# Optimization experiments

Measured on AMD Instinct MI355X. Metric: run time of the kernel, lower is better.

Reference implementation:

```python
import jax, jax.numpy as jnp
import numpy as np

B, H, S, E = 4, 8, 2048, 640
HD = E // H          # 80
MULT = 6
CHUNK = 128          # chunk size for the chunked-recurrent linear attention

def _alibi_slopes(n):
    # standard ALiBi slopes for power-of-2 n (matches _build_slope_tensor)
    start = 2.0 ** (-(2.0 ** -(np.log2(n) - 3.0)))
    return np.array([start * (start ** i) for i in range(n)], dtype=np.float32)

def setup_inputs() -> dict:
    key = jax.random.key(0)
    ks = jax.random.split(key, 3)
    x = jax.random.normal(ks[0], (B, S, E), jnp.float32)
    W1 = jax.random.normal(ks[1], (HD, MULT * HD), jnp.float32) * 0.05
    b1 = jnp.zeros((MULT * HD,), jnp.float32)
    W2 = jax.random.normal(ks[2], (MULT * HD, HD), jnp.float32) * 0.05
    b2 = jnp.zeros((HD,), jnp.float32)
    gamma = jnp.ones((HD,), jnp.float32)
    beta = jnp.zeros((HD,), jnp.float32)
    slopes = jnp.asarray(_alibi_slopes(H))
    return {"x": x, "W1": W1, "b1": b1, "W2": W2, "b2": b2,
            "gamma": gamma, "beta": beta, "slopes": slopes}

def _ln(x, g, b, eps=1e-5):
    m = x.mean(-1, keepdims=True)
    v = x.var(-1, keepdims=True)
    return (x - m) * jax.lax.rsqrt(v + eps) * g + b

def _lightning_attn(q, k, v, s):
    # linear attention with per-head decay exp(-s*(t-i)), causal, no softmax.
    b, h, n, d = q.shape
    c = CHUNK
    nc = n // c
    t = jnp.arange(c, dtype=q.dtype)
    diff = t[:, None] - t[None, :]
    Dmat = jnp.where(diff >= 0, jnp.exp(-s[:, None, None] * diff), 0.0)  # (h,c,c)
    q_dec = jnp.exp(-s[:, None] * t)        # (h,c): decay of query vs chunk start
    k_dec = jnp.exp(-s[:, None] * (c - t))  # (h,c): decay of key to next chunk start
    blk = jnp.exp(-s * c)                   # (h,): whole-chunk state decay

    def to_chunks(a):
        return a.reshape(b, h, nc, c, d).transpose(2, 0, 1, 3, 4)  # (nc,b,h,c,d)

    qc, kc, vc = to_chunks(q), to_chunks(k), to_chunks(v)

    def step(kv, inp):
        qb, kb, vb = inp                                    # (b,h,c,d)
        sc = jnp.einsum('bhid,bhjd->bhij', qb, kb) * Dmat[None]
        o = jnp.einsum('bhij,bhjd->bhid', sc, vb)           # intra-chunk
        o = o + jnp.einsum('bhid,bhde->bhie', qb * q_dec[None, :, :, None], kv)
        kv = blk[None, :, None, None] * kv + jnp.einsum(
            'bhid,bhie->bhde', kb * k_dec[None, :, :, None], vb)
        return kv, o

    kv0 = jnp.zeros((b, h, d, d), q.dtype)
    _, outs = jax.lax.scan(step, kv0, (qc, kc, vc))          # (nc,b,h,c,d)
    return outs.transpose(1, 2, 0, 3, 4).reshape(b, h, n, d)

def reference(x, W1, b1, W2, b2, gamma, beta, slopes):
    hdn = x.reshape(B, H, S, HD)
    hdn = _ln(hdn, gamma, beta)
    residual = hdn  # fixed residual, per the original forward
    for _ in range(2):
        a = _lightning_attn(hdn, hdn, hdn, slopes)
        hdn = _ln(a + residual, gamma, beta)
        ff = jax.nn.leaky_relu(hdn @ W1 + b1) @ W2 + b2  # dropout = eval identity
        hdn = _ln(ff + residual, gamma, beta)
    return hdn.mean(axis=1)  # mean over heads -> (B, S, HD)
```

## Files before the change

kernel.cpp:

```cpp
#include <hip/hip_runtime.h>
#include <hip/hip_bf16.h>

#define BB 4
#define HH 8
#define SS 2048
#define HD 80
#define CC 128
#define NC 16
#define DH 480
#define NROW (BB*HH*SS)
#define ROWSZ ((size_t)NROW * HD)

typedef unsigned short ushortT;
typedef __attribute__((ext_vector_type(8))) short bfrag;
typedef __attribute__((ext_vector_type(4))) float f4;
typedef __attribute__((ext_vector_type(4))) unsigned int u4;

__device__ __forceinline__ ushortT f2bf(float f) {
    __hip_bfloat16 h = __float2bfloat16(f);
    ushortT u; __builtin_memcpy(&u, &h, 2); return u;
}
__device__ __forceinline__ float bf2f(ushortT u) {
    unsigned int x = ((unsigned int)u) << 16;
    float f; __builtin_memcpy(&f, &x, 4); return f;
}

__global__ __launch_bounds__(256) void k_prep(const float* __restrict__ W1,
                                              const float* __restrict__ W2,
                                              ushortT* __restrict__ W1T,
                                              ushortT* __restrict__ W2T) {
    int idx = blockIdx.x * 256 + threadIdx.x;
    if (idx < 480 * 96) {
        int n = idx / 96, k = idx - n * 96;
        float v = (k < HD) ? W1[k * DH + n] : 0.f;
        W1T[idx] = f2bf(v);
    } else if (idx < 480 * 96 + 80 * 480) {
        int j = idx - 480 * 96;
        int n = j / DH, k = j - n * DH;
        W2T[j] = f2bf(W2[k * HD + n]);
    }
}

__global__ __launch_bounds__(256) void k_ln0(const float* __restrict__ x,
                                             const float* __restrict__ g,
                                             const float* __restrict__ be,
                                             ushortT* __restrict__ hdnb,
                                             float* __restrict__ res) {
    int row  = blockIdx.x * 4 + (threadIdx.x >> 6);
    int lane = threadIdx.x & 63;
    const float* xr = x + (size_t)row * HD;
    float v0 = xr[lane];
    float v1 = (lane < 16) ? xr[64 + lane] : 0.f;
    float s  = v0 + v1;
    float sq = v0 * v0 + v1 * v1;
#pragma unroll
    for (int o = 32; o; o >>= 1) { s += __shfl_xor(s, o); sq += __shfl_xor(sq, o); }
    float m    = s * (1.f / 80.f);
    float var  = sq * (1.f / 80.f) - m * m;
    float rstd = rsqrtf(var + 1e-5f);
    size_t base = (size_t)row * HD;
    float y0 = (v0 - m) * rstd * g[lane] + be[lane];
    hdnb[base + lane] = f2bf(y0); res[base + lane] = y0;
    if (lane < 16) {
        float y1 = (v1 - m) * rstd * g[64 + lane] + be[64 + lane];
        hdnb[base + 64 + lane] = f2bf(y1); res[base + 64 + lane] = y1;
    }
}

__global__ __launch_bounds__(256) void k_attn_a(const ushortT* __restrict__ hdn,
                                                const float* __restrict__ slopes,
                                                float* __restrict__ oin,
                                                float* __restrict__ ckv) {
    __shared__ ushortT Xs[CC * 104];
    __shared__ ushortT SC[CC * 40];
    __shared__ ushortT XT[HD * 136];
    __shared__ float dec[CC];
    __shared__ float sqk[CC];

    int t    = threadIdx.x;
    int wave = t >> 6, lane = t & 63;
    int quad = lane >> 4, ln16 = lane & 15;
    int bk = blockIdx.x;
    int bh = bk >> 4;
    int n  = bk & 15;
    float sl = slopes[bh & 7];

    size_t chunkrow = (size_t)bh * SS + (size_t)n * CC;
    const ushortT* xb = hdn + chunkrow * HD;

    if (t < CC) {
        dec[t] = expf(-sl * (float)t);
        sqk[t] = expf(-0.5f * sl * (float)(CC - t));
    }
    for (int u = t; u < CC * HD; u += 256) {
        int i = u / HD, c = u - i * HD;
        ushortT v = xb[u];
        Xs[i * 104 + c] = v;
        XT[c * 136 + i] = v;
    }
    for (int u = t; u < CC * 16; u += 256) {
        int i = u >> 4, c = u & 15;
        Xs[i * 104 + 80 + c] = 0;
    }
    __syncthreads();

    bfrag a[2][3];
#pragma unroll
    for (int rt = 0; rt < 2; ++rt) {
        int mt = wave + rt * 4;
#pragma unroll
        for (int ks = 0; ks < 3; ++ks)
            a[rt][ks] = *(const bfrag*)&Xs[(mt * 16 + ln16) * 104 + ks * 32 + quad * 8];
    }

    f4 oacc[2][5];
#pragma unroll
    for (int rt = 0; rt < 2; ++rt)
#pragma unroll
        for (int ot = 0; ot < 5; ++ot) oacc[rt][ot] = (f4)0.f;

    for (int jt = 0; jt < 4; ++jt) {
        if (wave + 4 < 2 * jt) continue;
        int j0 = jt * 32;
        bfrag bq[2][3];
#pragma unroll
        for (int nt = 0; nt < 2; ++nt)
#pragma unroll
            for (int ks = 0; ks < 3; ++ks)
                bq[nt][ks] = *(const bfrag*)&Xs[(j0 + nt * 16 + ln16) * 104 + ks * 32 + quad * 8];

#pragma unroll
        for (int rt = 0; rt < 2; ++rt) {
            int mt = wave + rt * 4;
            if (mt < 2 * jt) continue;
            int i_base = mt * 16;
            f4 c0 = (f4)0.f, c1 = (f4)0.f;
#pragma unroll
            for (int ks = 0; ks < 3; ++ks) {
                c0 = __builtin_amdgcn_mfma_f32_16x16x32_bf16(a[rt][ks], bq[0][ks], c0, 0, 0, 0);
                c1 = __builtin_amdgcn_mfma_f32_16x16x32_bf16(a[rt][ks], bq[1][ks], c1, 0, 0, 0);
            }
#pragma unroll
            for (int r = 0; r < 4; ++r) {
                int i = i_base + quad * 4 + r;
                int d0 = i - (j0 + ln16);
                int d1 = d0 - 16;
                float f0 = (d0 >= 0) ? dec[d0] : 0.f;
                float f1 = (d1 >= 0) ? dec[d1] : 0.f;
                SC[i * 40 + ln16]      = f2bf(c0[r] * f0);
                SC[i * 40 + 16 + ln16] = f2bf(c1[r] * f1);
            }
            bfrag a2 = *(const bfrag*)&SC[(i_base + ln16) * 40 + quad * 8];
#pragma unroll
            for (int ot = 0; ot < 5; ++ot) {
                bfrag bv = *(const bfrag*)&XT[(ot * 16 + ln16) * 136 + j0 + quad * 8];
                oacc[rt][ot] = __builtin_amdgcn_mfma_f32_16x16x32_bf16(a2, bv, oacc[rt][ot], 0, 0, 0);
            }
        }
    }

#pragma unroll
    for (int rt = 0; rt < 2; ++rt) {
        int i_base = (wave + rt * 4) * 16;
#pragma unroll
        for (int r = 0; r < 4; ++r) {
            size_t grow = (chunkrow + i_base + quad * 4 + r) * HD;
#pragma unroll
            for (int ot = 0; ot < 5; ++ot)
                oin[grow + ot * 16 + ln16] = oacc[rt][ot][r];
        }
    }

    __syncthreads();
    for (int u = t; u < HD * CC; u += 256) {
        int e = u >> 7, j = u & 127;
        int idx = e * 136 + j;
        XT[idx] = f2bf(bf2f(XT[idx]) * sqk[j]);
    }
    __syncthreads();

    float* kvout = ckv + (size_t)bk * (HD * HD);
    for (int p = wave; p < 25; p += 4) {
        int me = p / 5, ne = p - me * 5;
        f4 c = (f4)0.f;
#pragma unroll
        for (int ks = 0; ks < 4; ++ks) {
            bfrag av = *(const bfrag*)&XT[(me * 16 + ln16) * 136 + ks * 32 + quad * 8];
            bfrag bv = *(const bfrag*)&XT[(ne * 16 + ln16) * 136 + ks * 32 + quad * 8];
            c = __builtin_amdgcn_mfma_f32_16x16x32_bf16(av, bv, c, 0, 0, 0);
        }
#pragma unroll
        for (int r = 0; r < 4; ++r)
            kvout[(me * 16 + quad * 4 + r) * HD + ne * 16 + ln16] = c[r];
    }
}

__global__ __launch_bounds__(256) void k_scan(float* __restrict__ kv,
                                              const float* __restrict__ slopes) {
    int idx = blockIdx.x * 256 + threadIdx.x;
    int bh  = idx / (HD * HD);
    int ed  = idx - bh * (HD * HD);
    float bd = expf(-slopes[bh & 7] * (float)CC);
    size_t base = (size_t)bh * NC * (HD * HD) + ed;
    float st = 0.f;
#pragma unroll
    for (int n = 0; n < NC; ++n) {
        size_t p = base + (size_t)n * (HD * HD);
        float cv = kv[p];
        kv[p] = st;
        st = bd * st + cv;
    }
}

__global__ __launch_bounds__(256) void k_attn_b(const ushortT* __restrict__ hdn_in,
                                                const float* __restrict__ oin,
                                                const float* __restrict__ kvs,
                                                const float* __restrict__ res,
                                                const float* __restrict__ slopes,
                                                const float* __restrict__ g,
                                                const float* __restrict__ be,
                                                ushortT* __restrict__ hdn_out) {
    __shared__ ushortT Qs[CC * 104];
    __shared__ ushortT KVT[80 * 104];

    int t    = threadIdx.x;
    int wave = t >> 6, lane = t & 63;
    int qd   = lane >> 4, ln16 = lane & 15;
    int bk = blockIdx.x;
    int bh = bk >> 4;
    int n  = bk & 15;
    float sl = slopes[bh & 7];

    size_t chunkrow = (size_t)bh * SS + (size_t)n * CC;
    const ushortT* xb = hdn_in + chunkrow * HD;
    const float* KV = kvs + ((size_t)bh * NC + n) * (HD * HD);

    {
        const u4* xin = (const u4*)xb;
        u4* Qs4 = (u4*)Qs;
        for (int u = t; u < CC * 10; u += 256) {
            int i = u / 10, c = u - i * 10;
            Qs4[i * 13 + c] = xin[u];
        }
        for (int u = t; u < CC * 16; u += 256) {
            int i = u >> 4, c = u & 15;
            Qs[i * 104 + 80 + c] = 0;
        }
    }
    for (int u = t; u < HD * HD; u += 256) {
        int e = u / HD, d = u - e * HD;
        KVT[d * 104 + e] = f2bf(KV[u]);
    }
    for (int u = t; u < HD * 16; u += 256) {
        int d = u >> 4, e = u & 15;
        KVT[d * 104 + 80 + e] = 0;
    }
    __syncthreads();

    int m0 = wave * 32;
    bfrag a[2][3];
#pragma unroll
    for (int rt = 0; rt < 2; ++rt)
#pragma unroll
        for (int ks = 0; ks < 3; ++ks)
            a[rt][ks] = *(const bfrag*)&Qs[(m0 + rt * 16 + ln16) * 104 + ks * 32 + qd * 8];

    f4 acc[2][5];
#pragma unroll
    for (int ot = 0; ot < 5; ++ot) {
#pragma unroll
        for (int rt = 0; rt < 2; ++rt) acc[rt][ot] = (f4)0.f;
#pragma unroll
        for (int ks = 0; ks < 3; ++ks) {
            bfrag b = *(const bfrag*)&KVT[(ot * 16 + ln16) * 104 + ks * 32 + qd * 8];
#pragma unroll
            for (int rt = 0; rt < 2; ++rt)
                acc[rt][ot] = __builtin_amdgcn_mfma_f32_16x16x32_bf16(a[rt][ks], b, acc[rt][ot], 0, 0, 0);
        }
    }

#pragma unroll
    for (int rt = 0; rt < 2; ++rt) {
#pragma unroll
        for (int r = 0; r < 4; ++r) {
            int i = m0 + rt * 16 + qd * 4 + r;
            float qdec = expf(-sl * (float)i);
            size_t grow = (chunkrow + i) * HD;
            float tv[5];
            float s = 0.f, sq = 0.f;
#pragma unroll
            for (int ot = 0; ot < 5; ++ot) {
                int col = ot * 16 + ln16;
                tv[ot] = oin[grow + col] + qdec * acc[rt][ot][r] + res[grow + col];
                s += tv[ot]; sq += tv[ot] * tv[ot];
            }
#pragma unroll
            for (int o = 8; o; o >>= 1) { s += __shfl_xor(s, o); sq += __shfl_xor(sq, o); }
            float m    = s * (1.f / 80.f);
            float var  = sq * (1.f / 80.f) - m * m;
            float rstd = rsqrtf(var + 1e-5f);
#pragma unroll
            for (int ot = 0; ot < 5; ++ot) {
                int col = ot * 16 + ln16;
                hdn_out[grow + col] = f2bf((tv[ot] - m) * rstd * g[col] + be[col]);
            }
        }
    }
}

__global__ __launch_bounds__(256, 2) void k_ffn(const ushortT* __restrict__ hdn_in,
                                                const ushortT* __restrict__ W1T,
                                                const float* __restrict__ b1,
                                                const ushortT* __restrict__ W2T,
                                                const float* __restrict__ b2,
                                                const float* __restrict__ res,
                                                const float* __restrict__ g,
                                                const float* __restrict__ be,
                                                ushortT* __restrict__ outb,
                                                float* __restrict__ outf,
                                                int write_f32) {
    __shared__ ushortT Xs[128 * 104];
    __shared__ ushortT WH[128 * 104];
    __shared__ ushortT W2s[80 * 104];

    int t    = threadIdx.x;
    int wave = t >> 6, lane = t & 63;
    int qd   = lane >> 4, ln16 = lane & 15;
    size_t rowbase = (size_t)blockIdx.x * 128;

    {
        const u4* xin = (const u4*)(hdn_in + rowbase * HD);
        u4* Xs4 = (u4*)Xs;
        for (int u = t; u < 128 * 10; u += 256) {
            int i = u / 10, c = u - i * 10;
            Xs4[i * 13 + c] = xin[u];
        }
        for (int u = t; u < 128 * 16; u += 256) {
            int i = u >> 4, c = u & 15;
            Xs[i * 104 + 80 + c] = 0;
        }
    }

    f4 acc[2][5];
#pragma unroll
    for (int rt = 0; rt < 2; ++rt)
#pragma unroll
        for (int ot = 0; ot < 5; ++ot) acc[rt][ot] = (f4)0.f;

    const u4* W1T16 = (const u4*)W1T;
    const u4* W2T16 = (const u4*)W2T;
    u4* WH16  = (u4*)WH;
    u4* W2s16 = (u4*)W2s;

    for (int jt = 0; jt < DH; jt += 96) {
        __syncthreads();
        for (int u = t; u < 96 * 12; u += 256) {
            int n = u / 12, k = u - n * 12;
            WH16[n * 13 + k] = W1T16[(size_t)(jt + n) * 12 + k];
        }
        for (int u = t; u < 80 * 12; u += 256) {
            int n = u / 12, k = u - n * 12;
            W2s16[n * 13 + k] = W2T16[(size_t)n * 60 + (jt >> 3) + k];
        }
        __syncthreads();

        f4 hc[2][6];
#pragma unroll
        for (int rt = 0; rt < 2; ++rt)
#pragma unroll
            for (int nt = 0; nt < 6; ++nt) hc[rt][nt] = (f4)0.f;
#pragma unroll
        for (int ks = 0; ks < 3; ++ks) {
            bfrag a0 = *(const bfrag*)&Xs[((wave * 2 + 0) * 16 + ln16) * 104 + ks * 32 + qd * 8];
            bfrag a1 = *(const bfrag*)&Xs[((wave * 2 + 1) * 16 + ln16) * 104 + ks * 32 + qd * 8];
#pragma unroll
            for (int nt = 0; nt < 6; ++nt) {
                bfrag b = *(const bfrag*)&WH[(nt * 16 + ln16) * 104 + ks * 32 + qd * 8];
                hc[0][nt] = __builtin_amdgcn_mfma_f32_16x16x32_bf16(a0, b, hc[0][nt], 0, 0, 0);
                hc[1][nt] = __builtin_amdgcn_mfma_f32_16x16x32_bf16(a1, b, hc[1][nt], 0, 0, 0);
            }
        }
        __syncthreads();

#pragma unroll
        for (int rt = 0; rt < 2; ++rt) {
            int mrow = (wave * 2 + rt) * 16 + qd * 4;
#pragma unroll
            for (int nt = 0; nt < 6; ++nt) {
                float bv = b1[jt + nt * 16 + ln16];
#pragma unroll
                for (int r = 0; r < 4; ++r) {
                    float v = hc[rt][nt][r] + bv;
                    v = (v > 0.f) ? v : 0.01f * v;
                    WH[(mrow + r) * 104 + nt * 16 + ln16] = f2bf(v);
                }
            }
        }
#pragma unroll
        for (int ks = 0; ks < 3; ++ks) {
            bfrag a0 = *(const bfrag*)&WH[((wave * 2 + 0) * 16 + ln16) * 104 + ks * 32 + qd * 8];
            bfrag a1 = *(const bfrag*)&WH[((wave * 2 + 1) * 16 + ln16) * 104 + ks * 32 + qd * 8];
#pragma unroll
            for (int ot = 0; ot < 5; ++ot) {
                bfrag b = *(const bfrag*)&W2s[(ot * 16 + ln16) * 104 + ks * 32 + qd * 8];
                acc[0][ot] = __builtin_amdgcn_mfma_f32_16x16x32_bf16(a0, b, acc[0][ot], 0, 0, 0);
                acc[1][ot] = __builtin_amdgcn_mfma_f32_16x16x32_bf16(a1, b, acc[1][ot], 0, 0, 0);
            }
        }
    }

#pragma unroll
    for (int rt = 0; rt < 2; ++rt) {
        int mbase = (wave * 2 + rt) * 16 + qd * 4;
#pragma unroll
        for (int r = 0; r < 4; ++r) {
            size_t row = rowbase + mbase + r;
            float tv[5];
            float s = 0.f, sq = 0.f;
#pragma unroll
            for (int ot = 0; ot < 5; ++ot) {
                int col = ot * 16 + ln16;
                tv[ot] = acc[rt][ot][r] + b2[col] + res[row * HD + col];
                s += tv[ot]; sq += tv[ot] * tv[ot];
            }
#pragma unroll
            for (int o = 8; o; o >>= 1) { s += __shfl_xor(s, o); sq += __shfl_xor(sq, o); }
            float m    = s * (1.f / 80.f);
            float var  = sq * (1.f / 80.f) - m * m;
            float rstd = rsqrtf(var + 1e-5f);
            if (write_f32) {
#pragma unroll
                for (int ot = 0; ot < 5; ++ot) {
                    int col = ot * 16 + ln16;
                    outf[row * HD + col] = (tv[ot] - m) * rstd * g[col] + be[col];
                }
            } else {
#pragma unroll
                for (int ot = 0; ot < 5; ++ot) {
                    int col = ot * 16 + ln16;
                    outb[row * HD + col] = f2bf((tv[ot] - m) * rstd * g[col] + be[col]);
                }
            }
        }
    }
}

__global__ __launch_bounds__(256) void k_mean(const float* __restrict__ hdn,
                                              float* __restrict__ out) {
    int idx = blockIdx.x * 256 + threadIdx.x;
    int b   = idx / (SS * HD);
    int sd  = idx - b * (SS * HD);
    float s = 0.f;
#pragma unroll
    for (int h = 0; h < HH; ++h)
        s += hdn[((size_t)(b * HH + h)) * (SS * HD) + sd];
    out[idx] = s * 0.125f;
}

extern "C" void kernel_launch(void* const* d_in, const int* in_sizes, int n_in,
                              void* d_out, int out_size, void* d_ws, size_t ws_size,
                              hipStream_t stream) {
    (void)in_sizes; (void)n_in; (void)out_size; (void)ws_size;
    const float* x      = (const float*)d_in[0];
    const float* W1     = (const float*)d_in[1];
    const float* b1     = (const float*)d_in[2];
    const float* W2     = (const float*)d_in[3];
    const float* b2     = (const float*)d_in[4];
    const float* gamma  = (const float*)d_in[5];
    const float* beta   = (const float*)d_in[6];
    const float* slopes = (const float*)d_in[7];
    float* out = (float*)d_out;
    float* ws  = (float*)d_ws;

    float*   res  = ws;
    ushortT* hdnb = (ushortT*)(ws + ROWSZ);
    float*   oin  = ws + 2 * ROWSZ;
    float*   kv   = ws + 3 * ROWSZ;
    float*   hdnf = ws + 4 * ROWSZ;

    ushortT* W1T = (ushortT*)d_out;
    ushortT* W2T = W1T + 480 * 96;

    k_prep<<<(480 * 96 + 80 * 480 + 255) / 256, 256, 0, stream>>>(W1, W2, W1T, W2T);
    k_ln0<<<NROW / 4, 256, 0, stream>>>(x, gamma, beta, hdnb, res);
    for (int it = 0; it < 2; ++it) {
        k_attn_a<<<BB * HH * NC, 256, 0, stream>>>(hdnb, slopes, oin, kv);
        k_scan<<<(BB * HH * HD * HD) / 256, 256, 0, stream>>>(kv, slopes);
        k_attn_b<<<BB * HH * NC, 256, 0, stream>>>(hdnb, oin, kv, res, slopes, gamma, beta, hdnb);
        k_ffn<<<NROW / 128, 256, 0, stream>>>(hdnb, W1T, b1, W2T, b2, res, gamma, beta,
                                              hdnb, hdnf, (it == 1) ? 1 : 0);
    }
    k_mean<<<(BB * SS * HD) / 256, 256, 0, stream>>>(hdnf, out);
}
```

Baseline: 232.7 us.

## Fuse inter-chunk KV prefix scan into attention kernel and vectorize head mean

Removes the separate k_scan kernel. Each k_attn_b block now recomputes its decayed prefix state by summing all earlier chunk KV contributions itself (O(n) reads per block), then transposes the result into LDS. This saves one launch and a read-write pass over the KV buffer, but adds redundant global reads that grow with chunk index, about 8x the KV traffic on average. k_mean is also vectorized to float4 loads and stores with a quarter as many threads.

Result: slower. 258.4 us (+11.0%).

```diff
diff --git a/kernel.cpp b/kernel.cpp
--- a/kernel.cpp
+++ b/kernel.cpp
@@ -195,26 +195,9 @@
     }
 }
 
-__global__ __launch_bounds__(256) void k_scan(float* __restrict__ kv,
-                                              const float* __restrict__ slopes) {
-    int idx = blockIdx.x * 256 + threadIdx.x;
-    int bh  = idx / (HD * HD);
-    int ed  = idx - bh * (HD * HD);
-    float bd = expf(-slopes[bh & 7] * (float)CC);
-    size_t base = (size_t)bh * NC * (HD * HD) + ed;
-    float st = 0.f;
-#pragma unroll
-    for (int n = 0; n < NC; ++n) {
-        size_t p = base + (size_t)n * (HD * HD);
-        float cv = kv[p];
-        kv[p] = st;
-        st = bd * st + cv;
-    }
-}
-
 __global__ __launch_bounds__(256) void k_attn_b(const ushortT* __restrict__ hdn_in,
                                                 const float* __restrict__ oin,
-                                                const float* __restrict__ kvs,
+                                                const float* __restrict__ ckv,
                                                 const float* __restrict__ res,
                                                 const float* __restrict__ slopes,
                                                 const float* __restrict__ g,
@@ -233,7 +216,6 @@
 
     size_t chunkrow = (size_t)bh * SS + (size_t)n * CC;
     const ushortT* xb = hdn_in + chunkrow * HD;
-    const float* KV = kvs + ((size_t)bh * NC + n) * (HD * HD);
 
     {
         const u4* xin = (const u4*)xb;
@@ -247,13 +229,37 @@
             Qs[i * 104 + 80 + c] = 0;
         }
     }
-    for (int u = t; u < HD * HD; u += 256) {
-        int e = u / HD, d = u - e * HD;
-        KVT[d * 104 + e] = f2bf(KV[u]);
-    }
-    for (int u = t; u < HD * 16; u += 256) {
-        int d = u >> 4, e = u & 15;
-        KVT[d * 104 + 80 + e] = 0;
+
+    {
+        float bd = expf(-sl * (float)CC);
+        f4 acc4[7];
+#pragma unroll
+        for (int k = 0; k < 7; ++k) acc4[k] = (f4)0.f;
+        const f4* cb = (const f4*)(ckv + (size_t)bh * NC * (HD * HD));
+        for (int m = 0; m < n; ++m) {
+            const f4* cm = cb + (size_t)m * 1600;
+#pragma unroll
+            for (int k = 0; k < 7; ++k) {
+                int u = t + 256 * k;
+                if (u < 1600) acc4[k] = bd * acc4[k] + cm[u];
+            }
+        }
+#pragma unroll
+        for (int k = 0; k < 7; ++k) {
+            int u = t + 256 * k;
+            if (u < 1600) {
+                int jb = u * 4;
+#pragma unroll
+                for (int z = 0; z < 4; ++z) {
+                    int j = jb + z, e = j / 80, d = j - e * 80;
+                    KVT[d * 104 + e] = f2bf(acc4[k][z]);
+                }
+            }
+        }
+        for (int u = t; u < HD * 16; u += 256) {
+            int d = u >> 4, e = u & 15;
+            KVT[d * 104 + 80 + e] = 0;
+        }
     }
     __syncthreads();
 
@@ -448,13 +454,16 @@
 __global__ __launch_bounds__(256) void k_mean(const float* __restrict__ hdn,
                                               float* __restrict__ out) {
     int idx = blockIdx.x * 256 + threadIdx.x;
-    int b   = idx / (SS * HD);
-    int sd  = idx - b * (SS * HD);
-    float s = 0.f;
-#pragma unroll
-    for (int h = 0; h < HH; ++h)
-        s += hdn[((size_t)(b * HH + h)) * (SS * HD) + sd];
-    out[idx] = s * 0.125f;
+    int b   = idx / (SS * HD / 4);
+    int sd  = idx - b * (SS * HD / 4);
+    const f4* hp = (const f4*)hdn;
+    f4 s = (f4)0.f;
+#pragma unroll
+    for (int h = 0; h < HH; ++h) {
+        f4 v = hp[(size_t)(b * HH + h) * (SS * HD / 4) + sd];
+        s = s + v;
+    }
+    ((f4*)out)[idx] = s * 0.125f;
 }
 
 extern "C" void kernel_launch(void* const* d_in, const int* in_sizes, int n_in,
@@ -475,7 +484,7 @@
     float*   res  = ws;
     ushortT* hdnb = (ushortT*)(ws + ROWSZ);
     float*   oin  = ws + 2 * ROWSZ;
-    float*   kv   = ws + 3 * ROWSZ;
+    float*   ckv  = ws + 3 * ROWSZ;
     float*   hdnf = ws + 4 * ROWSZ;
 
     ushortT* W1T = (ushortT*)d_out;
@@ -484,11 +493,10 @@
     k_prep<<<(480 * 96 + 80 * 480 + 255) / 256, 256, 0, stream>>>(W1, W2, W1T, W2T);
     k_ln0<<<NROW / 4, 256, 0, stream>>>(x, gamma, beta, hdnb, res);
     for (int it = 0; it < 2; ++it) {
-        k_attn_a<<<BB * HH * NC, 256, 0, stream>>>(hdnb, slopes, oin, kv);
-        k_scan<<<(BB * HH * HD * HD) / 256, 256, 0, stream>>>(kv, slopes);
-        k_attn_b<<<BB * HH * NC, 256, 0, stream>>>(hdnb, oin, kv, res, slopes, gamma, beta, hdnb);
+        k_attn_a<<<BB * HH * NC, 256, 0, stream>>>(hdnb, slopes, oin, ckv);
+        k_attn_b<<<BB * HH * NC, 256, 0, stream>>>(hdnb, oin, ckv, res, slopes, gamma, beta, hdnb);
         k_ffn<<<NROW / 128, 256, 0, stream>>>(hdnb, W1T, b1, W2T, b2, res, gamma, beta,
                                               hdnb, hdnf, (it == 1) ? 1 : 0);
     }
-    k_mean<<<(BB * SS * HD) / 256, 256, 0, stream>>>(hdnf, out);
-}
+    k_mean<<<(BB * SS * HD) / (256 * 4), 256, 0, stream>>>(hdnf, out);
+}
```
